# Kernel optimization log

Hardware: AMD Instinct MI355X
Metric: run time of the kernel (lower is better)

The kernel has to match this reference:

```python
import jax, jax.numpy as jnp
import numpy as np
from jax import lax

NUM_DISP = 64
BLOCK = 21
EPS = 1e-12  # F.normalize default eps


def _box_sum(v):
    # v: (N, H, W) -> BLOCK x BLOCK zero-padded box sum (same shape), separable.
    p = BLOCK // 2
    v = v[:, None]  # (N,1,H,W)
    kv = jnp.ones((1, 1, BLOCK, 1), v.dtype)
    kh = jnp.ones((1, 1, 1, BLOCK), v.dtype)
    v = lax.conv_general_dilated(v, kv, (1, 1), ((p, p), (0, 0)))
    v = lax.conv_general_dilated(v, kh, (1, 1), ((0, 0), (p, p)))
    return v[:, 0]


def _l2norm_c(img):
    n = jnp.sqrt(jnp.sum(img * img, axis=1, keepdims=True))
    return img / jnp.maximum(n, EPS)


def _disparity(left, right):
    # left, right: (B, 3, H, W)
    left = _l2norm_c(left)
    right = _l2norm_c(right)
    B, C, H, W = left.shape
    d = jnp.arange(NUM_DISP)
    xs = jnp.arange(W)
    idx = xs[None, :] - d[:, None]              # (D, W): source column in right image
    valid = (idx >= 0)
    r_shift = right[:, :, :, jnp.clip(idx, 0)]  # (B, C, H, D, W)
    r_shift = jnp.where(valid[None, None, None], r_shift, 0.0)
    # per-pixel channel-summed absolute difference -> (B, D, H, W)
    diff = jnp.sum(jnp.abs(left[:, :, :, None, :] - r_shift), axis=1)  # (B, H, D, W)
    diff = jnp.transpose(diff, (0, 2, 1, 3))    # (B, D, H, W)
    cost = _box_sum(diff.reshape(B * NUM_DISP, H, W)).reshape(B, NUM_DISP, H, W)
    cost = cost / (C * BLOCK * BLOCK)           # mean SAD over block elements
    return jnp.argmin(cost, axis=1).astype(left.dtype)  # (B, H, W)


def setup_inputs() -> dict:
    key = jax.random.key(0)
    k1, k2 = jax.random.split(key)
    x = jax.random.normal(k1, (2, 6, 320, 512), dtype=jnp.float32)
    gt = jax.random.normal(k2, (2, 6, 320, 512), dtype=jnp.float32)
    return {"x": x, "gt": gt}


def reference(x, gt):
    disp_gt = _disparity(gt[:, :3], gt[:, 3:])
    disp_pred = _disparity(x[:, :3], x[:, 3:])
    return jnp.mean(jnp.abs(disp_pred - disp_gt))
```

## Files before the change

### kernel.cpp

```cpp
#include <hip/hip_runtime.h>
#include <math.h>

constexpr int B = 2, H = 320, W = 512, D = 64;
constexpr int HW = H * W;
constexpr int R = 10;
constexpr int SEG = 80;
constexpr int NSEG = H / SEG;
constexpr int RS = 548;
constexpr float EPS = 1e-12f;

__global__ void k_norm(const float* __restrict__ x, const float* __restrict__ gt,
                       float4* __restrict__ nrm4) {
    int idx = blockIdx.x * 256 + threadIdx.x;
    if (idx >= 2 * B * (HW / 4)) return;
    int t = idx / (B * (HW / 4));
    int rem = idx - t * (B * (HW / 4));
    int b = rem / (HW / 4);
    int hw4 = rem - b * (HW / 4);
    const float* p = (t == 0 ? x : gt) + (size_t)b * 6 * HW + 4 * hw4;
    float4 c[6];
#pragma unroll
    for (int ch = 0; ch < 6; ++ch) c[ch] = *(const float4*)(p + (size_t)ch * HW);
    float4* q = nrm4 + (size_t)(t * B + b) * 2 * HW + 4 * hw4;
    float4 o0[4], o1[4];
    const float* cf = (const float*)c;
#pragma unroll
    for (int k = 0; k < 4; ++k) {
        float v0 = cf[k], v1 = cf[4 + k], v2 = cf[8 + k];
        float v3 = cf[12 + k], v4 = cf[16 + k], v5 = cf[20 + k];
        float n1 = fmaxf(sqrtf(v0 * v0 + v1 * v1 + v2 * v2), EPS);
        float n2 = fmaxf(sqrtf(v3 * v3 + v4 * v4 + v5 * v5), EPS);
        o0[k] = make_float4(v0 / n1, v1 / n1, v2 / n1, 0.f);
        o1[k] = make_float4(v3 / n2, v4 / n2, v5 / n2, 0.f);
    }
#pragma unroll
    for (int k = 0; k < 4; ++k) { q[k] = o0[k]; q[HW + k] = o1[k]; }
}

template<bool FUSE>
__global__ __launch_bounds__(512, 2) void k_cost(const float4* __restrict__ nrm4,
                                                 float* __restrict__ cost,
                                                 const float* __restrict__ cprev,
                                                 float* __restrict__ dprev, int t) {
    const int blk = blockIdx.x;
    const int combo = blk & 7;
    const int d = blk >> 3;
    const int b = combo >> 2;
    const int seg = combo & 3;
    const int w = threadIdx.x;
    const float4* L4 = nrm4 + (size_t)(t * B + b) * 2 * HW;
    const float4* R4 = L4 + HW;
    const bool val = (w >= d);
    const int wr = val ? (w - d) : 0;
    const int h0 = seg * SEG;

    __shared__ float ring[21][W];
    __shared__ float vsb[2][8][RS];
    {
        int j = w >> 6, k = w & 63;
        if (k < 10)      { vsb[0][j][k] = 0.f;       vsb[1][j][k] = 0.f; }
        else if (k < 20) { vsb[0][j][512 + k] = 0.f; vsb[1][j][512 + k] = 0.f; }
    }

    auto diff = [&](int h) -> float {
        float4 l = L4[(size_t)h * W + w];
        if (val) {
            float4 r = R4[(size_t)h * W + wr];
            return fabsf(l.x - r.x) + fabsf(l.y - r.y) + fabsf(l.z - r.z);
        }
        return fabsf(l.x) + fabsf(l.y) + fabsf(l.z);
    };

    float vs = 0.f;
    for (int k = 0; k < 20; ++k) {
        int h = h0 - R + k;
        float dv0 = (h >= 0) ? diff(h) : 0.f;
        ring[k][w] = dv0;
        vs += dv0;
    }
    ring[20][w] = 0.f;

    const float* cp0 = nullptr; const float* cp1 = nullptr;
    int px0 = 0, px1 = 0;
    float best0 = 3.4e38f, best1 = 3.4e38f;
    int bd0 = 0, bd1 = 0;
    if (FUSE) {
        px0 = blk * 640 + w;
        int b0 = (px0 >= HW) ? 1 : 0;
        cp0 = cprev + (size_t)b0 * D * HW + (px0 - b0 * HW);
        if (w < 128) {
            px1 = blk * 640 + 512 + w;
            int b1 = (px1 >= HW) ? 1 : 0;
            cp1 = cprev + (size_t)b1 * D * HW + (px1 - b1 * HW);
        }
    }

    const int cc = threadIdx.x >> 3;
    const int jj = threadIdx.x & 7;
    float* cp = cost + ((size_t)(b * D + d) * H) * W;

    int slot0 = 20;
    int dc = 0;
    for (int ss = 0; ss < 10; ++ss) {
        const int nd = (ss < 4) ? 7 : 6;
        int sl[8];
        float dold[8], dv[8];
#pragma unroll
        for (int j = 0; j < 8; ++j) { int s2 = slot0 + j; if (s2 >= 21) s2 -= 21; sl[j] = s2; }
#pragma unroll
        for (int j = 0; j < 8; ++j) dold[j] = ring[sl[j]][w];
#pragma unroll
        for (int j = 0; j < 8; ++j) {
            int hn = h0 + ss * 8 + j + R;
            dv[j] = (hn < H) ? diff(hn) : 0.f;
        }
        float fv0[7], fv1[7];
        if (FUSE) {
#pragma unroll
            for (int q = 0; q < 7; ++q)
                if (q < nd) fv0[q] = cp0[(size_t)(dc + q) * HW];
            if (w < 128) {
#pragma unroll
                for (int q = 0; q < 7; ++q)
                    if (q < nd) fv1[q] = cp1[(size_t)(dc + q) * HW];
            }
        }
#pragma unroll
        for (int j = 0; j < 8; ++j) ring[sl[j]][w] = dv[j];
        float* vrow = &vsb[ss & 1][0][0];
#pragma unroll
        for (int j = 0; j < 8; ++j) { vs += dv[j] - dold[j]; vrow[j * RS + 10 + w] = vs; }
        __syncthreads();
        const float* vp = &vsb[ss & 1][jj][8 * cc];
        float wnd[28];
#pragma unroll
        for (int q = 0; q < 7; ++q) {
            float4 v4 = *(const float4*)(vp + 4 * q);
            wnd[4 * q] = v4.x; wnd[4 * q + 1] = v4.y;
            wnd[4 * q + 2] = v4.z; wnd[4 * q + 3] = v4.w;
        }
        float o = 0.f;
#pragma unroll
        for (int k = 0; k < 21; ++k) o += wnd[k];
        float out[8];
        out[0] = o;
#pragma unroll
        for (int k = 1; k < 8; ++k) { o += wnd[20 + k] - wnd[k - 1]; out[k] = o; }
        float* op = cp + (size_t)(h0 + ss * 8 + jj) * W + 8 * cc;
        *(float4*)(op)     = make_float4(out[0], out[1], out[2], out[3]);
        *(float4*)(op + 4) = make_float4(out[4], out[5], out[6], out[7]);
        if (FUSE) {
#pragma unroll
            for (int q = 0; q < 7; ++q)
                if (q < nd && fv0[q] < best0) { best0 = fv0[q]; bd0 = dc + q; }
            if (w < 128) {
#pragma unroll
                for (int q = 0; q < 7; ++q)
                    if (q < nd && fv1[q] < best1) { best1 = fv1[q]; bd1 = dc + q; }
            }
        }
        dc += nd;
        slot0 += 8; if (slot0 >= 21) slot0 -= 21;
    }
    if (FUSE) {
        dprev[px0] = (float)bd0;
        if (w < 128) dprev[px1] = (float)bd1;
    }
}

__global__ void k_amin(const float* __restrict__ cost, float* __restrict__ disp) {
    int blk = blockIdx.x;
    int b = (blk * 1024 >= HW) ? 1 : 0;
    int hw0 = blk * 1024 - b * HW + threadIdx.x * 4;
    const float* cp = cost + (size_t)b * D * HW + hw0;
    float4 v = *(const float4*)cp;
    float bb[4] = {v.x, v.y, v.z, v.w};
    int bd[4] = {0, 0, 0, 0};
    for (int d = 1; d < D; ++d) {
        v = *(const float4*)(cp + (size_t)d * HW);
        if (v.x < bb[0]) { bb[0] = v.x; bd[0] = d; }
        if (v.y < bb[1]) { bb[1] = v.y; bd[1] = d; }
        if (v.z < bb[2]) { bb[2] = v.z; bd[2] = d; }
        if (v.w < bb[3]) { bb[3] = v.w; bd[3] = d; }
    }
    *(float4*)(disp + (size_t)blk * 1024 + threadIdx.x * 4) =
        make_float4((float)bd[0], (float)bd[1], (float)bd[2], (float)bd[3]);
}

__global__ void k_fin(const float* __restrict__ cost1, const float* __restrict__ disp0,
                      float* __restrict__ part) {
    int blk = blockIdx.x;
    int b = (blk * 1024 >= HW) ? 1 : 0;
    int hw0 = blk * 1024 - b * HW + threadIdx.x * 4;
    const float* cp = cost1 + (size_t)b * D * HW + hw0;
    float4 v = *(const float4*)cp;
    float bb[4] = {v.x, v.y, v.z, v.w};
    int bd[4] = {0, 0, 0, 0};
    for (int d = 1; d < D; ++d) {
        v = *(const float4*)(cp + (size_t)d * HW);
        if (v.x < bb[0]) { bb[0] = v.x; bd[0] = d; }
        if (v.y < bb[1]) { bb[1] = v.y; bd[1] = d; }
        if (v.z < bb[2]) { bb[2] = v.z; bd[2] = d; }
        if (v.w < bb[3]) { bb[3] = v.w; bd[3] = d; }
    }
    float4 d0 = *(const float4*)(disp0 + (size_t)blk * 1024 + threadIdx.x * 4);
    float s = fabsf((float)bd[0] - d0.x) + fabsf((float)bd[1] - d0.y) +
              fabsf((float)bd[2] - d0.z) + fabsf((float)bd[3] - d0.w);
    __shared__ float sm[256];
    sm[threadIdx.x] = s;
    __syncthreads();
    for (int off = 128; off; off >>= 1) {
        if (threadIdx.x < off) sm[threadIdx.x] += sm[threadIdx.x + off];
        __syncthreads();
    }
    if (!threadIdx.x) part[blockIdx.x] = sm[0];
}

__global__ void k_red2(const float* __restrict__ part, float* __restrict__ out,
                       int nb, float inv) {
    __shared__ float sm[256];
    int tid = threadIdx.x;
    float s = 0.f;
    for (int i = tid; i < nb; i += 256) s += part[i];
    sm[tid] = s;
    __syncthreads();
    for (int off = 128; off; off >>= 1) {
        if (tid < off) sm[tid] += sm[tid + off];
        __syncthreads();
    }
    if (!tid) out[0] = sm[0] * inv;
}

extern "C" void kernel_launch(void* const* d_in, const int* in_sizes, int n_in,
                              void* d_out, int out_size, void* d_ws, size_t ws_size,
                              hipStream_t stream) {
    const float* x  = (const float*)d_in[0];
    const float* gt = (const float*)d_in[1];

    constexpr size_t NRM_F4 = (size_t)2 * B * 2 * HW;
    constexpr size_t COST_F = (size_t)B * D * HW;
    constexpr int AMIN_BLKS = B * HW / 1024;
    constexpr int NRM_BLKS  = (2 * B * (HW / 4) + 255) / 256;

    float4* nrm4 = (float4*)d_ws;
    float* cost0 = (float*)(nrm4 + NRM_F4);

    size_t need_primary = NRM_F4 * 16 + 2 * COST_F * 4 + (size_t)(B * HW + 4096) * 4;

    k_norm<<<NRM_BLKS, 256, 0, stream>>>(x, gt, nrm4);

    if (ws_size >= need_primary) {
        float* cost1 = cost0 + COST_F;
        float* disp0 = cost1 + COST_F;
        float* part  = disp0 + (size_t)B * HW;
        k_cost<false><<<B * NSEG * D, 512, 0, stream>>>(nrm4, cost0, nullptr, nullptr, 0);
        k_cost<true><<<B * NSEG * D, 512, 0, stream>>>(nrm4, cost1, cost0, disp0, 1);
        k_fin<<<AMIN_BLKS, 256, 0, stream>>>(cost1, disp0, part);
        k_red2<<<1, 256, 0, stream>>>(part, (float*)d_out, AMIN_BLKS, 1.f / (float)(B * HW));
    } else {
        float* disp0 = cost0 + COST_F;
        float* part  = disp0 + (size_t)B * HW;
        k_cost<false><<<B * NSEG * D, 512, 0, stream>>>(nrm4, cost0, nullptr, nullptr, 0);
        k_amin<<<AMIN_BLKS, 256, 0, stream>>>(cost0, disp0);
        k_cost<false><<<B * NSEG * D, 512, 0, stream>>>(nrm4, cost0, nullptr, nullptr, 1);
        k_fin<<<AMIN_BLKS, 256, 0, stream>>>(cost0, disp0, part);
        k_red2<<<1, 256, 0, stream>>>(part, (float*)d_out, AMIN_BLKS, 1.f / (float)(B * HW));
    }
}
```

Before: 193.6 us.

## Split final argmin into parallel disparity chunks with packed keys; prefetch diff rows

```diff
diff --git a/kernel.cpp b/kernel.cpp
--- a/kernel.cpp
+++ b/kernel.cpp
@@ -7,11 +7,13 @@
 constexpr int SEG = 80;
 constexpr int NSEG = H / SEG;
 constexpr int RS = 548;
+constexpr int QUADS = B * HW / 4;
 constexpr float EPS = 1e-12f;
+constexpr unsigned KM = 0xFFFFFFC0u;
 
 __global__ void k_norm(const float* __restrict__ x, const float* __restrict__ gt,
                        float4* __restrict__ nrm4) {
-    int idx = blockIdx.x * 256 + threadIdx.x;
+    int idx = blockIdx.x * 128 + threadIdx.x;
     if (idx >= 2 * B * (HW / 4)) return;
     int t = idx / (B * (HW / 4));
     int rem = idx - t * (B * (HW / 4));
@@ -99,21 +101,23 @@
     const int jj = threadIdx.x & 7;
     float* cp = cost + ((size_t)(b * D + d) * H) * W;
 
+    float dvv[8];
+#pragma unroll
+    for (int j = 0; j < 8; ++j) {
+        int hn = h0 + j + R;
+        dvv[j] = (hn < H) ? diff(hn) : 0.f;
+    }
+
     int slot0 = 20;
     int dc = 0;
     for (int ss = 0; ss < 10; ++ss) {
         const int nd = (ss < 4) ? 7 : 6;
         int sl[8];
-        float dold[8], dv[8];
+        float dold[8];
 #pragma unroll
         for (int j = 0; j < 8; ++j) { int s2 = slot0 + j; if (s2 >= 21) s2 -= 21; sl[j] = s2; }
 #pragma unroll
         for (int j = 0; j < 8; ++j) dold[j] = ring[sl[j]][w];
-#pragma unroll
-        for (int j = 0; j < 8; ++j) {
-            int hn = h0 + ss * 8 + j + R;
-            dv[j] = (hn < H) ? diff(hn) : 0.f;
-        }
         float fv0[7], fv1[7];
         if (FUSE) {
 #pragma unroll
@@ -126,10 +130,21 @@
             }
         }
 #pragma unroll
-        for (int j = 0; j < 8; ++j) ring[sl[j]][w] = dv[j];
+        for (int j = 0; j < 8; ++j) ring[sl[j]][w] = dvv[j];
         float* vrow = &vsb[ss & 1][0][0];
 #pragma unroll
-        for (int j = 0; j < 8; ++j) { vs += dv[j] - dold[j]; vrow[j * RS + 10 + w] = vs; }
+        for (int j = 0; j < 8; ++j) { vs += dvv[j] - dold[j]; vrow[j * RS + 10 + w] = vs; }
+        float dvn[8];
+        if (ss < 9) {
+#pragma unroll
+            for (int j = 0; j < 8; ++j) {
+                int hn = h0 + (ss + 1) * 8 + j + R;
+                dvn[j] = (hn < H) ? diff(hn) : 0.f;
+            }
+        } else {
+#pragma unroll
+            for (int j = 0; j < 8; ++j) dvn[j] = 0.f;
+        }
         __syncthreads();
         const float* vp = &vsb[ss & 1][jj][8 * cc];
         float wnd[28];
@@ -159,6 +174,8 @@
                     if (q < nd && fv1[q] < best1) { best1 = fv1[q]; bd1 = dc + q; }
             }
         }
+#pragma unroll
+        for (int j = 0; j < 8; ++j) dvv[j] = dvn[j];
         dc += nd;
         slot0 += 8; if (slot0 >= 21) slot0 -= 21;
     }
@@ -166,6 +183,57 @@
         dprev[px0] = (float)bd0;
         if (w < 128) dprev[px1] = (float)bd1;
     }
+}
+
+__global__ void k_aminA(const float* __restrict__ cost, uint4* __restrict__ keys) {
+    int idx = blockIdx.x * 256 + threadIdx.x;
+    int c = idx / QUADS;
+    int q = idx - c * QUADS;
+    int b = q / (QUADS / B);
+    int ql = q - b * (QUADS / B);
+    const float* cp = cost + (size_t)b * D * HW + 4 * ql;
+    int d0 = c * 16;
+    float4 v = *(const float4*)(cp + (size_t)d0 * HW);
+    unsigned kx = (__float_as_uint(v.x) & KM) | (unsigned)d0;
+    unsigned ky = (__float_as_uint(v.y) & KM) | (unsigned)d0;
+    unsigned kz = (__float_as_uint(v.z) & KM) | (unsigned)d0;
+    unsigned kw = (__float_as_uint(v.w) & KM) | (unsigned)d0;
+#pragma unroll 4
+    for (int k = 1; k < 16; ++k) {
+        unsigned d = (unsigned)(d0 + k);
+        v = *(const float4*)(cp + (size_t)(d0 + k) * HW);
+        unsigned e;
+        e = (__float_as_uint(v.x) & KM) | d; kx = (e < kx) ? e : kx;
+        e = (__float_as_uint(v.y) & KM) | d; ky = (e < ky) ? e : ky;
+        e = (__float_as_uint(v.z) & KM) | d; kz = (e < kz) ? e : kz;
+        e = (__float_as_uint(v.w) & KM) | d; kw = (e < kw) ? e : kw;
+    }
+    keys[idx] = make_uint4(kx, ky, kz, kw);
+}
+
+__global__ void k_aminB(const uint4* __restrict__ keys, const float* __restrict__ disp0,
+                        float* __restrict__ part) {
+    int q = blockIdx.x * 256 + threadIdx.x;
+    uint4 m = keys[q];
+#pragma unroll
+    for (int c = 1; c < 4; ++c) {
+        uint4 kc = keys[(size_t)c * QUADS + q];
+        m.x = (kc.x < m.x) ? kc.x : m.x;
+        m.y = (kc.y < m.y) ? kc.y : m.y;
+        m.z = (kc.z < m.z) ? kc.z : m.z;
+        m.w = (kc.w < m.w) ? kc.w : m.w;
+    }
+    float4 d0 = *(const float4*)(disp0 + (size_t)4 * q);
+    float s = fabsf((float)(m.x & 63u) - d0.x) + fabsf((float)(m.y & 63u) - d0.y) +
+              fabsf((float)(m.z & 63u) - d0.z) + fabsf((float)(m.w & 63u) - d0.w);
+    __shared__ float sm[256];
+    sm[threadIdx.x] = s;
+    __syncthreads();
+    for (int off = 128; off; off >>= 1) {
+        if (threadIdx.x < off) sm[threadIdx.x] += sm[threadIdx.x + off];
+        __syncthreads();
+    }
+    if (!threadIdx.x) part[blockIdx.x] = sm[0];
 }
 
 __global__ void k_amin(const float* __restrict__ cost, float* __restrict__ disp) {
@@ -187,35 +255,6 @@
         make_float4((float)bd[0], (float)bd[1], (float)bd[2], (float)bd[3]);
 }
 
-__global__ void k_fin(const float* __restrict__ cost1, const float* __restrict__ disp0,
-                      float* __restrict__ part) {
-    int blk = blockIdx.x;
-    int b = (blk * 1024 >= HW) ? 1 : 0;
-    int hw0 = blk * 1024 - b * HW + threadIdx.x * 4;
-    const float* cp = cost1 + (size_t)b * D * HW + hw0;
-    float4 v = *(const float4*)cp;
-    float bb[4] = {v.x, v.y, v.z, v.w};
-    int bd[4] = {0, 0, 0, 0};
-    for (int d = 1; d < D; ++d) {
-        v = *(const float4*)(cp + (size_t)d * HW);
-        if (v.x < bb[0]) { bb[0] = v.x; bd[0] = d; }
-        if (v.y < bb[1]) { bb[1] = v.y; bd[1] = d; }
-        if (v.z < bb[2]) { bb[2] = v.z; bd[2] = d; }
-        if (v.w < bb[3]) { bb[3] = v.w; bd[3] = d; }
-    }
-    float4 d0 = *(const float4*)(disp0 + (size_t)blk * 1024 + threadIdx.x * 4);
-    float s = fabsf((float)bd[0] - d0.x) + fabsf((float)bd[1] - d0.y) +
-              fabsf((float)bd[2] - d0.z) + fabsf((float)bd[3] - d0.w);
-    __shared__ float sm[256];
-    sm[threadIdx.x] = s;
-    __syncthreads();
-    for (int off = 128; off; off >>= 1) {
-        if (threadIdx.x < off) sm[threadIdx.x] += sm[threadIdx.x + off];
-        __syncthreads();
-    }
-    if (!threadIdx.x) part[blockIdx.x] = sm[0];
-}
-
 __global__ void k_red2(const float* __restrict__ part, float* __restrict__ out,
                        int nb, float inv) {
     __shared__ float sm[256];
@@ -239,31 +278,35 @@
 
     constexpr size_t NRM_F4 = (size_t)2 * B * 2 * HW;
     constexpr size_t COST_F = (size_t)B * D * HW;
-    constexpr int AMIN_BLKS = B * HW / 1024;
-    constexpr int NRM_BLKS  = (2 * B * (HW / 4) + 255) / 256;
+    constexpr int NRM_BLKS  = (2 * B * (HW / 4) + 127) / 128;
 
     float4* nrm4 = (float4*)d_ws;
     float* cost0 = (float*)(nrm4 + NRM_F4);
 
-    size_t need_primary = NRM_F4 * 16 + 2 * COST_F * 4 + (size_t)(B * HW + 4096) * 4;
-
-    k_norm<<<NRM_BLKS, 256, 0, stream>>>(x, gt, nrm4);
+    size_t need_primary = NRM_F4 * 16 + 2 * COST_F * 4 +
+                          (size_t)4 * QUADS * 16 + (size_t)(B * HW + 4096) * 4;
+
+    k_norm<<<NRM_BLKS, 128, 0, stream>>>(x, gt, nrm4);
 
     if (ws_size >= need_primary) {
         float* cost1 = cost0 + COST_F;
-        float* disp0 = cost1 + COST_F;
+        uint4* kd    = (uint4*)(cost1 + COST_F);
+        float* disp0 = (float*)(kd + (size_t)4 * QUADS);
         float* part  = disp0 + (size_t)B * HW;
         k_cost<false><<<B * NSEG * D, 512, 0, stream>>>(nrm4, cost0, nullptr, nullptr, 0);
         k_cost<true><<<B * NSEG * D, 512, 0, stream>>>(nrm4, cost1, cost0, disp0, 1);
-        k_fin<<<AMIN_BLKS, 256, 0, stream>>>(cost1, disp0, part);
-        k_red2<<<1, 256, 0, stream>>>(part, (float*)d_out, AMIN_BLKS, 1.f / (float)(B * HW));
+        k_aminA<<<4 * QUADS / 256, 256, 0, stream>>>(cost1, kd);
+        k_aminB<<<QUADS / 256, 256, 0, stream>>>(kd, disp0, part);
+        k_red2<<<1, 256, 0, stream>>>(part, (float*)d_out, QUADS / 256, 1.f / (float)(B * HW));
     } else {
         float* disp0 = cost0 + COST_F;
-        float* part  = disp0 + (size_t)B * HW;
+        uint4* kd    = (uint4*)(disp0 + (size_t)B * HW);
+        float* part  = (float*)(kd + (size_t)4 * QUADS);
         k_cost<false><<<B * NSEG * D, 512, 0, stream>>>(nrm4, cost0, nullptr, nullptr, 0);
-        k_amin<<<AMIN_BLKS, 256, 0, stream>>>(cost0, disp0);
+        k_amin<<<B * HW / 1024, 256, 0, stream>>>(cost0, disp0);
         k_cost<false><<<B * NSEG * D, 512, 0, stream>>>(nrm4, cost0, nullptr, nullptr, 1);
-        k_fin<<<AMIN_BLKS, 256, 0, stream>>>(cost0, disp0, part);
-        k_red2<<<1, 256, 0, stream>>>(part, (float*)d_out, AMIN_BLKS, 1.f / (float)(B * HW));
-    }
-}
+        k_aminA<<<4 * QUADS / 256, 256, 0, stream>>>(cost0, kd);
+        k_aminB<<<QUADS / 256, 256, 0, stream>>>(kd, disp0, part);
+        k_red2<<<1, 256, 0, stream>>>(part, (float*)d_out, QUADS / 256, 1.f / (float)(B * HW));
+    }
+}
```

After: 195.8 us. Within noise of the previous version (+1.1%).
